# Kernel tuning notes

Hardware: AMD Instinct MI355X
Metric: run time of the kernel (lower is better)

## Reference

```python
import jax, jax.numpy as jnp
import numpy as np

D_MODEL, D_K, D_V, H = 1024, 64, 64, 16
B, N = 4, 2048


def setup_inputs() -> dict:
    key = jax.random.key(0)
    ks = jax.random.split(key, 11)
    s = 0.02
    return {
        "Q": jax.random.normal(ks[0], (B, N, D_MODEL), jnp.float32),
        "K": jax.random.normal(ks[1], (B, N, D_MODEL), jnp.float32),
        "V": jax.random.normal(ks[2], (B, N, D_MODEL), jnp.float32),
        # stacked per-head projection weights: [h, d_model, d_k]
        "Wq": jax.random.normal(ks[3], (H, D_MODEL, D_K), jnp.float32) * s,
        "bq": jax.random.normal(ks[4], (H, D_K), jnp.float32) * s,
        "Wk": jax.random.normal(ks[5], (H, D_MODEL, D_K), jnp.float32) * s,
        "bk": jax.random.normal(ks[6], (H, D_K), jnp.float32) * s,
        "Wv": jax.random.normal(ks[7], (H, D_MODEL, D_V), jnp.float32) * s,
        "bv": jax.random.normal(ks[8], (H, D_V), jnp.float32) * s,
        "Wo": jax.random.normal(ks[9], (H * D_V, D_MODEL), jnp.float32) * s,
        "bo": jax.random.normal(ks[10], (D_MODEL,), jnp.float32) * s,
        "apply_mask": 1,
    }


def reference(Q, K, V, Wq, bq, Wk, bk, Wv, bv, Wo, bo, apply_mask):
    # fused per-head projections: [b, h, n, d_k]
    q = jnp.einsum("bnd,hdk->bhnk", Q, Wq) + bq[None, :, None, :]
    k = jnp.einsum("bnd,hdk->bhnk", K, Wk) + bk[None, :, None, :]
    v = jnp.einsum("bnd,hdv->bhnv", V, Wv) + bv[None, :, None, :]
    scores = jnp.einsum("bhnk,bhmk->bhnm", q, k) / jnp.sqrt(
        jnp.asarray(D_K, q.dtype)
    )
    if apply_mask:
        n = Q.shape[1]
        causal = jnp.tril(jnp.ones((n, n), dtype=bool))
        scores = jnp.where(causal[None, None], scores, -jnp.inf)
    weights = jax.nn.softmax(scores, axis=-1)
    out = jnp.einsum("bhnm,bhmv->bhnv", weights, v)
    # concat heads: [b, n, h*d_v]
    out = out.transpose(0, 2, 1, 3).reshape(Q.shape[0], Q.shape[1], H * D_V)
    return out @ Wo + bo
```

## Files before the change

### kernel.cpp

```cpp
#include <hip/hip_runtime.h>
#include <hip/hip_bf16.h>

#define H 16
#define DM 1024
#define DK 64
#define B_ 4
#define N_ 2048

typedef __attribute__((ext_vector_type(8))) short bf16x8;
typedef __attribute__((ext_vector_type(4))) short s16x4;
typedef __attribute__((ext_vector_type(2))) unsigned int u32x2;
typedef __attribute__((ext_vector_type(4))) float f32x4;

static __device__ __forceinline__ short f2bs(float x) {
    __hip_bfloat16 b = __float2bfloat16(x);
    return *reinterpret_cast<short*>(&b);
}

static __device__ __forceinline__ void async16(const void* g, void* l) {
    __builtin_amdgcn_global_load_lds(
        (const __attribute__((address_space(1))) void*)g,
        (__attribute__((address_space(3))) void*)l, 16, 0, 0);
}

static __device__ __forceinline__ unsigned packbf(float lo, float hi) {
    return __builtin_amdgcn_perm(__float_as_uint(hi), __float_as_uint(lo), 0x07060302u);
}

__global__ __launch_bounds__(256) void prep_kernel(
    const float* __restrict__ Q, const float* __restrict__ K, const float* __restrict__ V,
    const float* __restrict__ Wq, const float* __restrict__ Wk,
    const float* __restrict__ Wv, const float* __restrict__ Wo,
    short* __restrict__ Qb, short* __restrict__ Kb, short* __restrict__ Vb,
    short* __restrict__ wqT, short* __restrict__ wkT,
    short* __restrict__ wvT, short* __restrict__ woT)
{
    int y = blockIdx.y;
    if (y < 3) {
        const float* s = (y == 0) ? Q : (y == 1) ? K : V;
        short* d = (y == 0) ? Qb : (y == 1) ? Kb : Vb;
        size_t i = ((size_t)blockIdx.x * 256 + threadIdx.x) * 8;
        f32x4 a = *(const f32x4*)(s + i);
        f32x4 b = *(const f32x4*)(s + i + 4);
        bf16x8 p;
        #pragma unroll
        for (int j = 0; j < 4; ++j) { p[j] = f2bs(a[j]); p[4 + j] = f2bs(b[j]); }
        *(bf16x8*)(d + i) = p;
        return;
    }
    if (blockIdx.x >= 1024) return;
    __shared__ float tile[64][65];
    int z = blockIdx.x >> 8;
    int bx = blockIdx.x & 255;
    int t = threadIdx.x;
    int tj = t & 63, ti = t >> 6;

    if (z < 3) {
        const float* src = (z == 0) ? Wq : (z == 1) ? Wk : Wv;
        short* dst = (z == 0) ? wqT : (z == 1) ? wkT : wvT;
        int h = bx >> 4;
        int dmt = bx & 15;
        #pragma unroll
        for (int r = 0; r < 16; ++r) {
            int i = r * 4 + ti;
            tile[i][tj] = src[((size_t)h * 1024 + dmt * 64 + i) * 64 + tj];
        }
        __syncthreads();
        #pragma unroll
        for (int r = 0; r < 16; ++r) {
            int dk = r * 4 + ti;
            dst[((size_t)h * 64 + dk) * 1024 + dmt * 64 + tj] = f2bs(tile[tj][dk]);
        }
    } else {
        int kt = bx >> 4;
        int nt = bx & 15;
        #pragma unroll
        for (int r = 0; r < 16; ++r) {
            int i = r * 4 + ti;
            tile[i][tj] = Wo[((size_t)kt * 64 + i) * 1024 + nt * 64 + tj];
        }
        __syncthreads();
        #pragma unroll
        for (int r = 0; r < 16; ++r) {
            int jn = r * 4 + ti;
            woT[((size_t)nt * 64 + jn) * 1024 + kt * 64 + tj] = f2bs(tile[tj][jn]);
        }
    }
}

static __device__ __forceinline__ void gemm_mainloop(
    const short* __restrict__ A, const short* __restrict__ BT,
    int rowM0, int colN0, char* lds, f32x4 (&acc)[4][4])
{
    int tid = threadIdx.x;
    int lane = tid & 63, w = tid >> 6;
    int l16 = lane & 15, quad = lane >> 4;
    int wm = w >> 1, wn = w & 1;
    int xg = (quad ^ ((l16 >> 1) & 3)) << 4;

    int r0 = w * 32 + (lane >> 2);
    int gsl = ((lane & 3) ^ ((lane >> 3) & 3)) << 4;
    int dst0 = w * 2048 + lane * 16;
    const char* Ag0 = (const char*)A + (size_t)(rowM0 + r0) * 2048 + gsl;
    const char* Ag1 = Ag0 + 16 * 2048;
    const char* Bg0 = (const char*)BT + (size_t)(colN0 + r0) * 2048 + gsl;
    const char* Bg1 = Bg0 + 16 * 2048;

    #pragma unroll
    for (int t = 0; t < 2; ++t) {
        size_t kb = (size_t)t * 64;
        char* As = lds + t * 16384;
        char* Bs = As + 8192;
        async16(Ag0 + kb, As + dst0);
        async16(Ag1 + kb, As + dst0 + 1024);
        async16(Bg0 + kb, Bs + dst0);
        async16(Bg1 + kb, Bs + dst0 + 1024);
    }

    int c0 = 0;
    int cr = 32768;
    for (int it = 0; it < 32; ++it) {
        if (it < 31) asm volatile("s_waitcnt vmcnt(4)" ::: "memory");
        else         asm volatile("s_waitcnt vmcnt(0)" ::: "memory");
        __builtin_amdgcn_s_barrier();
        __builtin_amdgcn_sched_barrier(0);

        if (it + 2 < 32) {
            size_t kb = (size_t)(it + 2) * 64;
            char* Aw = lds + cr;
            char* Bw = Aw + 8192;
            async16(Ag0 + kb, Aw + dst0);
            async16(Ag1 + kb, Aw + dst0 + 1024);
            async16(Bg0 + kb, Bw + dst0);
            async16(Bg1 + kb, Bw + dst0 + 1024);
        }
        __builtin_amdgcn_sched_barrier(0);

        const char* As = lds + c0;
        const char* Bs = As + 8192;
        bf16x8 a[4], b[4];
        #pragma unroll
        for (int i = 0; i < 4; ++i)
            a[i] = *(const bf16x8*)(As + (wm * 64 + i * 16 + l16) * 64 + xg);
        #pragma unroll
        for (int j = 0; j < 4; ++j)
            b[j] = *(const bf16x8*)(Bs + (wn * 64 + j * 16 + l16) * 64 + xg);
        #pragma unroll
        for (int i = 0; i < 4; ++i)
            #pragma unroll
            for (int j = 0; j < 4; ++j)
                acc[i][j] = __builtin_amdgcn_mfma_f32_16x16x32_bf16(a[i], b[j], acc[i][j], 0, 0, 0);

        c0 += 16384; if (c0 == 49152) c0 = 0;
        cr += 16384; if (cr == 49152) cr = 0;
    }
}

__global__ __launch_bounds__(256) void proj_gemm(
    const short* __restrict__ Qb, const short* __restrict__ Kb, const short* __restrict__ Vb,
    const short* __restrict__ wqT, const short* __restrict__ wkT, const short* __restrict__ wvT,
    const float* __restrict__ bq, const float* __restrict__ bk, const float* __restrict__ bv,
    short* __restrict__ qbuf, short* __restrict__ kbuf, short* __restrict__ vTbuf)
{
    __shared__ char lds[49152];
    int id = blockIdx.x;
    int xcd = id & 7;
    int k = id >> 3;
    int which = k >> 6;
    int rem = k & 63;
    int r = ((rem >> 3) << 3) | xcd;
    int c = rem & 7;

    const short* A  = (which == 0) ? Qb : (which == 1) ? Kb : Vb;
    const short* BT = (which == 0) ? wqT : (which == 1) ? wkT : wvT;
    const float* bias = (which == 0) ? bq : (which == 1) ? bk : bv;

    int rowM0 = r * 128;
    int colN0 = c * 128;

    f32x4 acc[4][4];
    #pragma unroll
    for (int i = 0; i < 4; ++i)
        #pragma unroll
        for (int j = 0; j < 4; ++j) acc[i][j] = (f32x4){0.f, 0.f, 0.f, 0.f};

    gemm_mainloop(A, BT, rowM0, colN0, lds, acc);

    int lane = threadIdx.x & 63, w = threadIdx.x >> 6;
    int l16 = lane & 15, quad = lane >> 4;
    int wm = w >> 1, wn = w & 1;

    if (which == 2) {
        #pragma unroll
        for (int j = 0; j < 4; ++j) {
            int col = colN0 + wn * 64 + j * 16 + l16;
            int hh = col >> 6, dv = col & 63;
            float bs = bias[col];
            #pragma unroll
            for (int i = 0; i < 4; ++i) {
                int rowb = rowM0 + wm * 64 + i * 16 + quad * 4;
                int bb = rowb >> 11, n0 = rowb & 2047;
                s16x4 pk;
                #pragma unroll
                for (int r2 = 0; r2 < 4; ++r2) pk[r2] = f2bs(acc[i][j][r2] + bs);
                *(s16x4*)(vTbuf + (((size_t)bb * H + hh) * DK + dv) * N_ + n0) = pk;
            }
        }
    } else {
        short* dst = (which == 0) ? qbuf : kbuf;
        float scl = (which == 0) ? 0.180336880f : 1.0f;
        #pragma unroll
        for (int j = 0; j < 4; ++j) {
            int col = colN0 + wn * 64 + j * 16 + l16;
            float bs = bias[col];
            #pragma unroll
            for (int i = 0; i < 4; ++i) {
                int rowb = rowM0 + wm * 64 + i * 16 + quad * 4;
                #pragma unroll
                for (int r2 = 0; r2 < 4; ++r2)
                    dst[(size_t)(rowb + r2) * 1024 + col] = f2bs((acc[i][j][r2] + bs) * scl);
            }
        }
    }
}

__global__ __launch_bounds__(256) void out_gemm(
    const short* __restrict__ obuf, const short* __restrict__ woT,
    const float* __restrict__ bo, float* __restrict__ out)
{
    __shared__ char lds[49152];
    int id = blockIdx.x;
    int xcd = id & 7;
    int k = id >> 3;
    int r = ((k >> 3) << 3) | xcd;
    int c = k & 7;

    int rowM0 = r * 128;
    int colN0 = c * 128;

    f32x4 acc[4][4];
    #pragma unroll
    for (int i = 0; i < 4; ++i)
        #pragma unroll
        for (int j = 0; j < 4; ++j) acc[i][j] = (f32x4){0.f, 0.f, 0.f, 0.f};

    gemm_mainloop(obuf, woT, rowM0, colN0, lds, acc);

    int lane = threadIdx.x & 63, w = threadIdx.x >> 6;
    int l16 = lane & 15, quad = lane >> 4;
    int wm = w >> 1, wn = w & 1;

    #pragma unroll
    for (int j = 0; j < 4; ++j) {
        int col = colN0 + wn * 64 + j * 16 + l16;
        float bs = bo[col];
        #pragma unroll
        for (int i = 0; i < 4; ++i) {
            int rowb = rowM0 + wm * 64 + i * 16 + quad * 4;
            #pragma unroll
            for (int r2 = 0; r2 < 4; ++r2)
                out[(size_t)(rowb + r2) * 1024 + col] = acc[i][j][r2] + bs;
        }
    }
}

__global__ __launch_bounds__(256) void flash_kernel(
    const short* __restrict__ qbuf, const short* __restrict__ kbuf, const short* __restrict__ vT,
    short* __restrict__ obuf, const int* __restrict__ amask)
{
    __shared__ short Ks[2][4096];
    __shared__ short Vs[2][4096];
    __shared__ char  plds[4][2048];

    int bid = blockIdx.x;
    int g = bid & 7, idx = bid >> 3;
    int bh = g * 8 + (idx >> 4);
    int xq = idx & 15;
    int b = bh >> 4, h = bh & 15;

    int tid = threadIdx.x;
    int lane = tid & 63, wave = tid >> 6;
    int l16 = lane & 15, quad = lane >> 4;
    int msk = amask[0];

    int i8 = lane >> 3, i7 = lane & 7;
    int sg = (i7 ^ i8) << 4;
    int pk0 = i8 * 4 + wave;
    int skey = wave * 16 + i8;
    int ldst = wave * 2048 + lane * 16;

    const char* kbase = (const char*)(kbuf + (size_t)b * 2048 * 1024 + h * 64);
    const char* vbase = (const char*)(vT + ((size_t)(b * 16 + h) * 64) * 2048);

    int m7 = l16 & 7;
    int g0 = (quad ^ m7) << 4;
    int g1 = ((4 | quad) ^ m7) << 4;

    char* pw = plds[wave];
    int prd0 = l16 * 128 + g0;
    int prd1 = l16 * 128 + g1;
    int pwa[4];
    #pragma unroll
    for (int r = 0; r < 4; ++r) {
        int row = quad * 4 + r;
        pwa[r] = row * 128 + (((l16 >> 1) ^ (row & 7)) << 4) + ((l16 & 1) << 3);
    }

    for (int pass = 0; pass < 2; ++pass) {
        int qt = pass ? (31 - xq) : xq;
        int qw = qt * 64 + wave * 16;
        int nkb = msk ? (qt + 1) : 32;

        const short* qp = qbuf + ((size_t)(b * 2048 + qw + l16)) * 1024 + h * 64;
        bf16x8 aq0 = *(const bf16x8*)(qp + quad * 8);
        bf16x8 aq1 = *(const bf16x8*)(qp + 32 + quad * 8);

        f32x4 o[4];
        float lsum[4];
        #pragma unroll
        for (int i = 0; i < 4; ++i) { o[i] = (f32x4){0.f, 0.f, 0.f, 0.f}; lsum[i] = 0.f; }

        async16(kbase + (size_t)pk0 * 2048 + sg, (char*)Ks[0] + ldst);
        async16(kbase + (size_t)(pk0 + 32) * 2048 + sg, (char*)Ks[0] + ldst + 1024);
        async16(vbase + (size_t)skey * 4096 + sg, (char*)Vs[0] + ldst);
        async16(vbase + (size_t)(skey + 8) * 4096 + sg, (char*)Vs[0] + ldst + 1024);

        for (int ib = 0; ib < nkb; ++ib) {
            __syncthreads();
            int cur = ib & 1;
            if (ib + 1 < nkb) {
                int nb = (ib + 1) & 1;
                size_t kb2 = (size_t)(ib + 1) * 64;
                async16(kbase + (kb2 + pk0) * 2048 + sg, (char*)Ks[nb] + ldst);
                async16(kbase + (kb2 + pk0 + 32) * 2048 + sg, (char*)Ks[nb] + ldst + 1024);
                async16(vbase + (size_t)skey * 4096 + kb2 * 2 + sg, (char*)Vs[nb] + ldst);
                async16(vbase + (size_t)(skey + 8) * 4096 + kb2 * 2 + sg, (char*)Vs[nb] + ldst + 1024);
            }
            int kb = ib * 64;

            f32x4 s[4];
            __builtin_amdgcn_s_setprio(1);
            #pragma unroll
            for (int nt = 0; nt < 4; ++nt) {
                const char* kr = (const char*)Ks[cur] + (nt * 16 + l16) * 128;
                bf16x8 b0 = *(const bf16x8*)(kr + g0);
                bf16x8 b1 = *(const bf16x8*)(kr + g1);
                f32x4 t = (f32x4){0.f, 0.f, 0.f, 0.f};
                t = __builtin_amdgcn_mfma_f32_16x16x32_bf16(aq0, b0, t, 0, 0, 0);
                t = __builtin_amdgcn_mfma_f32_16x16x32_bf16(aq1, b1, t, 0, 0, 0);
                s[nt] = t;
            }
            __builtin_amdgcn_s_setprio(0);

            if (msk && (kb + 63 > qw)) {
                #pragma unroll
                for (int r = 0; r < 4; ++r) {
                    int row = qw + quad * 4 + r;
                    #pragma unroll
                    for (int nt = 0; nt < 4; ++nt) {
                        int col = kb + l16 * 4 + nt;
                        if (col > row) s[nt][r] = -3e38f;
                    }
                }
            }

            __builtin_amdgcn_wave_barrier();
            #pragma unroll
            for (int r = 0; r < 4; ++r) {
                float p0 = __builtin_amdgcn_exp2f(s[0][r]);
                float p1 = __builtin_amdgcn_exp2f(s[1][r]);
                float p2 = __builtin_amdgcn_exp2f(s[2][r]);
                float p3 = __builtin_amdgcn_exp2f(s[3][r]);
                lsum[r] += (p0 + p1) + (p2 + p3);
                u32x2 pk;
                pk[0] = packbf(p0, p1);
                pk[1] = packbf(p2, p3);
                *(u32x2*)(pw + pwa[r]) = pk;
            }
            __builtin_amdgcn_wave_barrier();
            bf16x8 ap0 = *(const bf16x8*)(pw + prd0);
            bf16x8 ap1 = *(const bf16x8*)(pw + prd1);
            __builtin_amdgcn_wave_barrier();

            __builtin_amdgcn_s_setprio(1);
            #pragma unroll
            for (int vb = 0; vb < 4; ++vb) {
                const char* vr = (const char*)Vs[cur] + (vb * 16 + l16) * 128;
                bf16x8 v0 = *(const bf16x8*)(vr + g0);
                bf16x8 v1 = *(const bf16x8*)(vr + g1);
                o[vb] = __builtin_amdgcn_mfma_f32_16x16x32_bf16(ap0, v0, o[vb], 0, 0, 0);
                o[vb] = __builtin_amdgcn_mfma_f32_16x16x32_bf16(ap1, v1, o[vb], 0, 0, 0);
            }
            __builtin_amdgcn_s_setprio(0);
        }

        #pragma unroll
        for (int r = 0; r < 4; ++r) {
            float t = lsum[r];
            #pragma unroll
            for (int off = 1; off < 16; off <<= 1) t += __shfl_xor(t, off, 64);
            float inv = 1.0f / t;
            int row = qw + quad * 4 + r;
            #pragma unroll
            for (int vb = 0; vb < 4; ++vb)
                obuf[((size_t)(b * 2048 + row)) * 1024 + h * 64 + vb * 16 + l16] =
                    f2bs(o[vb][r] * inv);
        }
        __syncthreads();
    }
}

extern "C" void kernel_launch(void* const* d_in, const int* in_sizes, int n_in,
                              void* d_out, int out_size, void* d_ws, size_t ws_size,
                              hipStream_t stream)
{
    const float* Q  = (const float*)d_in[0];
    const float* K  = (const float*)d_in[1];
    const float* V  = (const float*)d_in[2];
    const float* Wq = (const float*)d_in[3];
    const float* bq = (const float*)d_in[4];
    const float* Wk = (const float*)d_in[5];
    const float* bk = (const float*)d_in[6];
    const float* Wv = (const float*)d_in[7];
    const float* bv = (const float*)d_in[8];
    const float* Wo = (const float*)d_in[9];
    const float* bo = (const float*)d_in[10];
    const int* amask = (const int*)d_in[11];
    float* out = (float*)d_out;

    char* ws = (char*)d_ws;
    const size_t SZ = (size_t)B_ * N_ * DM * sizeof(short);
    const size_t SZW = (size_t)H * DK * DM * sizeof(short);
    short* Qb    = (short*)ws; ws += SZ;
    short* Kb    = (short*)ws; ws += SZ;
    short* Vb    = (short*)ws; ws += SZ;
    short* qbuf  = (short*)ws; ws += SZ;
    short* kbuf  = (short*)ws; ws += SZ;
    short* vTbuf = (short*)ws; ws += SZ;
    short* wqT   = (short*)ws; ws += SZW;
    short* wkT   = (short*)ws; ws += SZW;
    short* wvT   = (short*)ws; ws += SZW;
    short* woT   = (short*)ws; ws += SZW;
    short* obuf  = Qb;

    prep_kernel<<<dim3(4096, 4), dim3(256), 0, stream>>>(Q, K, V, Wq, Wk, Wv, Wo,
                                                         Qb, Kb, Vb, wqT, wkT, wvT, woT);
    proj_gemm<<<dim3(1536), dim3(256), 0, stream>>>(Qb, Kb, Vb, wqT, wkT, wvT,
                                                    bq, bk, bv, qbuf, kbuf, vTbuf);
    flash_kernel<<<dim3(1024), dim3(256), 0, stream>>>(qbuf, kbuf, vTbuf, obuf, amask);
    out_gemm<<<dim3(512), dim3(256), 0, stream>>>(obuf, woT, bo, out);
}
```

Measured before the change: 303.3 us.

## Fuse fp32-to-bf16 input conversion into projection GEMM mainloop

Removes the separate pass that converted Q, K and V from fp32 to bf16 into workspace. The projection GEMM now loads fp32 A tiles into registers, converts them to bf16 and writes them to LDS, with a one-stage register prefetch. The weight B tiles still use async global-to-LDS loads. This cuts a full read/write round trip of the activations, but adds conversion ALU work and register pressure inside the GEMM loop, and doubles the A bytes fetched per tile.

Measured after the change: 335.6 us. 10.7% more time.

```diff
diff --git a/kernel.cpp b/kernel.cpp
--- a/kernel.cpp
+++ b/kernel.cpp
@@ -27,28 +27,12 @@
     return __builtin_amdgcn_perm(__float_as_uint(hi), __float_as_uint(lo), 0x07060302u);
 }
 
-__global__ __launch_bounds__(256) void prep_kernel(
-    const float* __restrict__ Q, const float* __restrict__ K, const float* __restrict__ V,
+__global__ __launch_bounds__(256) void prep_w(
     const float* __restrict__ Wq, const float* __restrict__ Wk,
     const float* __restrict__ Wv, const float* __restrict__ Wo,
-    short* __restrict__ Qb, short* __restrict__ Kb, short* __restrict__ Vb,
     short* __restrict__ wqT, short* __restrict__ wkT,
     short* __restrict__ wvT, short* __restrict__ woT)
 {
-    int y = blockIdx.y;
-    if (y < 3) {
-        const float* s = (y == 0) ? Q : (y == 1) ? K : V;
-        short* d = (y == 0) ? Qb : (y == 1) ? Kb : Vb;
-        size_t i = ((size_t)blockIdx.x * 256 + threadIdx.x) * 8;
-        f32x4 a = *(const f32x4*)(s + i);
-        f32x4 b = *(const f32x4*)(s + i + 4);
-        bf16x8 p;
-        #pragma unroll
-        for (int j = 0; j < 4; ++j) { p[j] = f2bs(a[j]); p[4 + j] = f2bs(b[j]); }
-        *(bf16x8*)(d + i) = p;
-        return;
-    }
-    if (blockIdx.x >= 1024) return;
     __shared__ float tile[64][65];
     int z = blockIdx.x >> 8;
     int bx = blockIdx.x & 255;
@@ -85,6 +69,97 @@
             int jn = r * 4 + ti;
             woT[((size_t)nt * 64 + jn) * 1024 + kt * 64 + tj] = f2bs(tile[tj][jn]);
         }
+    }
+}
+
+static __device__ __forceinline__ void gemm_mainloop_f32A(
+    const float* __restrict__ Af, const short* __restrict__ BT,
+    int rowM0, int colN0, char* lds, f32x4 (&acc)[4][4])
+{
+    int tid = threadIdx.x;
+    int lane = tid & 63, w = tid >> 6;
+    int l16 = lane & 15, quad = lane >> 4;
+    int wm = w >> 1, wn = w & 1;
+    int xg = (quad ^ ((l16 >> 1) & 3)) << 4;
+
+    int r0 = w * 32 + (lane >> 2);
+    int gsl = ((lane & 3) ^ ((lane >> 3) & 3)) << 4;
+    int dst0 = w * 2048 + lane * 16;
+    const char* Af0 = (const char*)Af + (size_t)(rowM0 + r0) * 4096 + gsl * 2;
+    const char* Af1 = Af0 + (size_t)16 * 4096;
+    const char* Bg0 = (const char*)BT + (size_t)(colN0 + r0) * 2048 + gsl;
+    const char* Bg1 = Bg0 + 16 * 2048;
+
+    f32x4 c00, c01, c10, c11;
+
+    c00 = *(const f32x4*)(Af0);
+    c01 = *(const f32x4*)(Af0 + 16);
+    c10 = *(const f32x4*)(Af1);
+    c11 = *(const f32x4*)(Af1 + 16);
+    async16(Bg0, lds + 8192 + dst0);
+    async16(Bg1, lds + 8192 + dst0 + 1024);
+    {
+        bf16x8 p0, p1;
+        #pragma unroll
+        for (int j = 0; j < 4; ++j) {
+            p0[j] = f2bs(c00[j]); p0[4 + j] = f2bs(c01[j]);
+            p1[j] = f2bs(c10[j]); p1[4 + j] = f2bs(c11[j]);
+        }
+        *(bf16x8*)(lds + dst0) = p0;
+        *(bf16x8*)(lds + dst0 + 1024) = p1;
+    }
+    c00 = *(const f32x4*)(Af0 + 128);
+    c01 = *(const f32x4*)(Af0 + 144);
+    c10 = *(const f32x4*)(Af1 + 128);
+    c11 = *(const f32x4*)(Af1 + 144);
+    async16(Bg0 + 64, lds + 16384 + 8192 + dst0);
+    async16(Bg1 + 64, lds + 16384 + 8192 + dst0 + 1024);
+
+    int o0 = 0, o1 = 16384, o2 = 32768;
+    for (int it = 0; it < 32; ++it) {
+        if (it < 31) asm volatile("s_waitcnt vmcnt(6) lgkmcnt(0)" ::: "memory");
+        else         asm volatile("s_waitcnt vmcnt(0) lgkmcnt(0)" ::: "memory");
+        __builtin_amdgcn_s_barrier();
+        __builtin_amdgcn_sched_barrier(0);
+
+        if (it + 1 < 32) {
+            bf16x8 p0, p1;
+            #pragma unroll
+            for (int j = 0; j < 4; ++j) {
+                p0[j] = f2bs(c00[j]); p0[4 + j] = f2bs(c01[j]);
+                p1[j] = f2bs(c10[j]); p1[4 + j] = f2bs(c11[j]);
+            }
+            *(bf16x8*)(lds + o1 + dst0) = p0;
+            *(bf16x8*)(lds + o1 + dst0 + 1024) = p1;
+        }
+        if (it + 2 < 32) {
+            int fo = (it + 2) * 128;
+            c00 = *(const f32x4*)(Af0 + fo);
+            c01 = *(const f32x4*)(Af0 + fo + 16);
+            c10 = *(const f32x4*)(Af1 + fo);
+            c11 = *(const f32x4*)(Af1 + fo + 16);
+            int bo2 = (it + 2) * 64;
+            async16(Bg0 + bo2, lds + o2 + 8192 + dst0);
+            async16(Bg1 + bo2, lds + o2 + 8192 + dst0 + 1024);
+        }
+        __builtin_amdgcn_sched_barrier(0);
+
+        const char* As = lds + o0;
+        const char* Bs = As + 8192;
+        bf16x8 a[4], b[4];
+        #pragma unroll
+        for (int i = 0; i < 4; ++i)
+            a[i] = *(const bf16x8*)(As + (wm * 64 + i * 16 + l16) * 64 + xg);
+        #pragma unroll
+        for (int j = 0; j < 4; ++j)
+            b[j] = *(const bf16x8*)(Bs + (wn * 64 + j * 16 + l16) * 64 + xg);
+        #pragma unroll
+        for (int i = 0; i < 4; ++i)
+            #pragma unroll
+            for (int j = 0; j < 4; ++j)
+                acc[i][j] = __builtin_amdgcn_mfma_f32_16x16x32_bf16(a[i], b[j], acc[i][j], 0, 0, 0);
+
+        int tmp = o0; o0 = o1; o1 = o2; o2 = tmp;
     }
 }
 
@@ -157,7 +232,7 @@
 }
 
 __global__ __launch_bounds__(256) void proj_gemm(
-    const short* __restrict__ Qb, const short* __restrict__ Kb, const short* __restrict__ Vb,
+    const float* __restrict__ Qf, const float* __restrict__ Kf, const float* __restrict__ Vf,
     const short* __restrict__ wqT, const short* __restrict__ wkT, const short* __restrict__ wvT,
     const float* __restrict__ bq, const float* __restrict__ bk, const float* __restrict__ bv,
     short* __restrict__ qbuf, short* __restrict__ kbuf, short* __restrict__ vTbuf)
@@ -171,7 +246,7 @@
     int r = ((rem >> 3) << 3) | xcd;
     int c = rem & 7;
 
-    const short* A  = (which == 0) ? Qb : (which == 1) ? Kb : Vb;
+    const float* A  = (which == 0) ? Qf : (which == 1) ? Kf : Vf;
     const short* BT = (which == 0) ? wqT : (which == 1) ? wkT : wvT;
     const float* bias = (which == 0) ? bq : (which == 1) ? bk : bv;
 
@@ -184,7 +259,7 @@
         #pragma unroll
         for (int j = 0; j < 4; ++j) acc[i][j] = (f32x4){0.f, 0.f, 0.f, 0.f};
 
-    gemm_mainloop(A, BT, rowM0, colN0, lds, acc);
+    gemm_mainloop_f32A(A, BT, rowM0, colN0, lds, acc);
 
     int lane = threadIdx.x & 63, w = threadIdx.x >> 6;
     int l16 = lane & 15, quad = lane >> 4;
@@ -431,9 +506,7 @@
     char* ws = (char*)d_ws;
     const size_t SZ = (size_t)B_ * N_ * DM * sizeof(short);
     const size_t SZW = (size_t)H * DK * DM * sizeof(short);
-    short* Qb    = (short*)ws; ws += SZ;
-    short* Kb    = (short*)ws; ws += SZ;
-    short* Vb    = (short*)ws; ws += SZ;
+    short* obuf  = (short*)ws; ws += SZ;
     short* qbuf  = (short*)ws; ws += SZ;
     short* kbuf  = (short*)ws; ws += SZ;
     short* vTbuf = (short*)ws; ws += SZ;
@@ -441,11 +514,9 @@
     short* wkT   = (short*)ws; ws += SZW;
     short* wvT   = (short*)ws; ws += SZW;
     short* woT   = (short*)ws; ws += SZW;
-    short* obuf  = Qb;
-
-    prep_kernel<<<dim3(4096, 4), dim3(256), 0, stream>>>(Q, K, V, Wq, Wk, Wv, Wo,
-                                                         Qb, Kb, Vb, wqT, wkT, wvT, woT);
-    proj_gemm<<<dim3(1536), dim3(256), 0, stream>>>(Qb, Kb, Vb, wqT, wkT, wvT,
+
+    prep_w<<<dim3(1024), dim3(256), 0, stream>>>(Wq, Wk, Wv, Wo, wqT, wkT, wvT, woT);
+    proj_gemm<<<dim3(1536), dim3(256), 0, stream>>>(Q, K, V, wqT, wkT, wvT,
                                                     bq, bk, bv, qbuf, kbuf, vTbuf);
     flash_kernel<<<dim3(1024), dim3(256), 0, stream>>>(qbuf, kbuf, vTbuf, obuf, amask);
     out_gemm<<<dim3(512), dim3(256), 0, stream>>>(obuf, woT, bo, out);
```

## Share K/V tiles between paired causal query tiles; drop XCD-aware block remap

Applied to the files above, without the earlier changes.

The flash kernel previously ran two sequential passes per block, for query tile xq and then 31-xq, loading K/V tiles from global memory in each pass. It now processes both query tiles in a single loop over key blocks. Each loaded K/V tile is reused for the short tile as well while it is still in range, which removes the duplicate K/V loads and the extra barriers. This costs more registers, since two sets of accumulators and Q fragments are live at once, and that may lower occupancy. Separately, the GEMM kernels drop the XCD-swizzled block index mapping in favour of a plain 2D/3D grid, which may hurt L2 locality across XCDs.

Measured after the change: 328.0 us. 1.08x slower.

```diff
diff --git a/kernel.cpp b/kernel.cpp
--- a/kernel.cpp
+++ b/kernel.cpp
@@ -163,20 +163,13 @@
     short* __restrict__ qbuf, short* __restrict__ kbuf, short* __restrict__ vTbuf)
 {
     __shared__ char lds[49152];
-    int id = blockIdx.x;
-    int xcd = id & 7;
-    int k = id >> 3;
-    int which = k >> 6;
-    int rem = k & 63;
-    int r = ((rem >> 3) << 3) | xcd;
-    int c = rem & 7;
-
+    int which = blockIdx.z;
     const short* A  = (which == 0) ? Qb : (which == 1) ? Kb : Vb;
     const short* BT = (which == 0) ? wqT : (which == 1) ? wkT : wvT;
     const float* bias = (which == 0) ? bq : (which == 1) ? bk : bv;
 
-    int rowM0 = r * 128;
-    int colN0 = c * 128;
+    int rowM0 = blockIdx.x * 128;
+    int colN0 = blockIdx.y * 128;
 
     f32x4 acc[4][4];
     #pragma unroll
@@ -229,14 +222,8 @@
     const float* __restrict__ bo, float* __restrict__ out)
 {
     __shared__ char lds[49152];
-    int id = blockIdx.x;
-    int xcd = id & 7;
-    int k = id >> 3;
-    int r = ((k >> 3) << 3) | xcd;
-    int c = k & 7;
-
-    int rowM0 = r * 128;
-    int colN0 = c * 128;
+    int rowM0 = blockIdx.x * 128;
+    int colN0 = blockIdx.y * 128;
 
     f32x4 acc[4][4];
     #pragma unroll
@@ -306,38 +293,47 @@
         pwa[r] = row * 128 + (((l16 >> 1) ^ (row & 7)) << 4) + ((l16 & 1) << 3);
     }
 
-    for (int pass = 0; pass < 2; ++pass) {
-        int qt = pass ? (31 - xq) : xq;
-        int qw = qt * 64 + wave * 16;
-        int nkb = msk ? (qt + 1) : 32;
-
-        const short* qp = qbuf + ((size_t)(b * 2048 + qw + l16)) * 1024 + h * 64;
-        bf16x8 aq0 = *(const bf16x8*)(qp + quad * 8);
-        bf16x8 aq1 = *(const bf16x8*)(qp + 32 + quad * 8);
-
-        f32x4 o[4];
-        float lsum[4];
-        #pragma unroll
-        for (int i = 0; i < 4; ++i) { o[i] = (f32x4){0.f, 0.f, 0.f, 0.f}; lsum[i] = 0.f; }
-
-        async16(kbase + (size_t)pk0 * 2048 + sg, (char*)Ks[0] + ldst);
-        async16(kbase + (size_t)(pk0 + 32) * 2048 + sg, (char*)Ks[0] + ldst + 1024);
-        async16(vbase + (size_t)skey * 4096 + sg, (char*)Vs[0] + ldst);
-        async16(vbase + (size_t)(skey + 8) * 4096 + sg, (char*)Vs[0] + ldst + 1024);
-
-        for (int ib = 0; ib < nkb; ++ib) {
-            __syncthreads();
-            int cur = ib & 1;
-            if (ib + 1 < nkb) {
-                int nb = (ib + 1) & 1;
-                size_t kb2 = (size_t)(ib + 1) * 64;
-                async16(kbase + (kb2 + pk0) * 2048 + sg, (char*)Ks[nb] + ldst);
-                async16(kbase + (kb2 + pk0 + 32) * 2048 + sg, (char*)Ks[nb] + ldst + 1024);
-                async16(vbase + (size_t)skey * 4096 + kb2 * 2 + sg, (char*)Vs[nb] + ldst);
-                async16(vbase + (size_t)(skey + 8) * 4096 + kb2 * 2 + sg, (char*)Vs[nb] + ldst + 1024);
-            }
-            int kb = ib * 64;
-
+    int qtA = xq, qtB = 31 - xq;
+    int qwA = qtA * 64 + wave * 16;
+    int qwB = qtB * 64 + wave * 16;
+    int nkbA = msk ? (qtA + 1) : 32;
+    int nkbB = msk ? (qtB + 1) : 32;
+
+    const short* qpA = qbuf + ((size_t)(b * 2048 + qwA + l16)) * 1024 + h * 64;
+    const short* qpB = qbuf + ((size_t)(b * 2048 + qwB + l16)) * 1024 + h * 64;
+    bf16x8 aqA0 = *(const bf16x8*)(qpA + quad * 8);
+    bf16x8 aqA1 = *(const bf16x8*)(qpA + 32 + quad * 8);
+    bf16x8 aqB0 = *(const bf16x8*)(qpB + quad * 8);
+    bf16x8 aqB1 = *(const bf16x8*)(qpB + 32 + quad * 8);
+
+    f32x4 oA[4], oB[4];
+    float lsA[4], lsB[4];
+    #pragma unroll
+    for (int i = 0; i < 4; ++i) {
+        oA[i] = (f32x4){0.f, 0.f, 0.f, 0.f};
+        oB[i] = (f32x4){0.f, 0.f, 0.f, 0.f};
+        lsA[i] = 0.f; lsB[i] = 0.f;
+    }
+
+    async16(kbase + (size_t)pk0 * 2048 + sg, (char*)Ks[0] + ldst);
+    async16(kbase + (size_t)(pk0 + 32) * 2048 + sg, (char*)Ks[0] + ldst + 1024);
+    async16(vbase + (size_t)skey * 4096 + sg, (char*)Vs[0] + ldst);
+    async16(vbase + (size_t)(skey + 8) * 4096 + sg, (char*)Vs[0] + ldst + 1024);
+
+    for (int ib = 0; ib < nkbB; ++ib) {
+        __syncthreads();
+        int cur = ib & 1;
+        if (ib + 1 < nkbB) {
+            int nb = (ib + 1) & 1;
+            size_t kb2 = (size_t)(ib + 1) * 64;
+            async16(kbase + (kb2 + pk0) * 2048 + sg, (char*)Ks[nb] + ldst);
+            async16(kbase + (kb2 + pk0 + 32) * 2048 + sg, (char*)Ks[nb] + ldst + 1024);
+            async16(vbase + (size_t)skey * 4096 + kb2 * 2 + sg, (char*)Vs[nb] + ldst);
+            async16(vbase + (size_t)(skey + 8) * 4096 + kb2 * 2 + sg, (char*)Vs[nb] + ldst + 1024);
+        }
+        int kb = ib * 64;
+
+        {
             f32x4 s[4];
             __builtin_amdgcn_s_setprio(1);
             #pragma unroll
@@ -346,16 +342,16 @@
                 bf16x8 b0 = *(const bf16x8*)(kr + g0);
                 bf16x8 b1 = *(const bf16x8*)(kr + g1);
                 f32x4 t = (f32x4){0.f, 0.f, 0.f, 0.f};
-                t = __builtin_amdgcn_mfma_f32_16x16x32_bf16(aq0, b0, t, 0, 0, 0);
-                t = __builtin_amdgcn_mfma_f32_16x16x32_bf16(aq1, b1, t, 0, 0, 0);
+                t = __builtin_amdgcn_mfma_f32_16x16x32_bf16(aqB0, b0, t, 0, 0, 0);
+                t = __builtin_amdgcn_mfma_f32_16x16x32_bf16(aqB1, b1, t, 0, 0, 0);
                 s[nt] = t;
             }
             __builtin_amdgcn_s_setprio(0);
 
-            if (msk && (kb + 63 > qw)) {
+            if (msk && (kb + 63 > qwB)) {
                 #pragma unroll
                 for (int r = 0; r < 4; ++r) {
-                    int row = qw + quad * 4 + r;
+                    int row = qwB + quad * 4 + r;
                     #pragma unroll
                     for (int nt = 0; nt < 4; ++nt) {
                         int col = kb + l16 * 4 + nt;
@@ -371,7 +367,7 @@
                 float p1 = __builtin_amdgcn_exp2f(s[1][r]);
                 float p2 = __builtin_amdgcn_exp2f(s[2][r]);
                 float p3 = __builtin_amdgcn_exp2f(s[3][r]);
-                lsum[r] += (p0 + p1) + (p2 + p3);
+                lsB[r] += (p0 + p1) + (p2 + p3);
                 u32x2 pk;
                 pk[0] = packbf(p0, p1);
                 pk[1] = packbf(p2, p3);
@@ -388,25 +384,93 @@
                 const char* vr = (const char*)Vs[cur] + (vb * 16 + l16) * 128;
                 bf16x8 v0 = *(const bf16x8*)(vr + g0);
                 bf16x8 v1 = *(const bf16x8*)(vr + g1);
-                o[vb] = __builtin_amdgcn_mfma_f32_16x16x32_bf16(ap0, v0, o[vb], 0, 0, 0);
-                o[vb] = __builtin_amdgcn_mfma_f32_16x16x32_bf16(ap1, v1, o[vb], 0, 0, 0);
+                oB[vb] = __builtin_amdgcn_mfma_f32_16x16x32_bf16(ap0, v0, oB[vb], 0, 0, 0);
+                oB[vb] = __builtin_amdgcn_mfma_f32_16x16x32_bf16(ap1, v1, oB[vb], 0, 0, 0);
             }
             __builtin_amdgcn_s_setprio(0);
         }
 
-        #pragma unroll
-        for (int r = 0; r < 4; ++r) {
-            float t = lsum[r];
-            #pragma unroll
-            for (int off = 1; off < 16; off <<= 1) t += __shfl_xor(t, off, 64);
-            float inv = 1.0f / t;
-            int row = qw + quad * 4 + r;
-            #pragma unroll
-            for (int vb = 0; vb < 4; ++vb)
-                obuf[((size_t)(b * 2048 + row)) * 1024 + h * 64 + vb * 16 + l16] =
-                    f2bs(o[vb][r] * inv);
-        }
-        __syncthreads();
+        if (ib < nkbA) {
+            f32x4 s[4];
+            __builtin_amdgcn_s_setprio(1);
+            #pragma unroll
+            for (int nt = 0; nt < 4; ++nt) {
+                const char* kr = (const char*)Ks[cur] + (nt * 16 + l16) * 128;
+                bf16x8 b0 = *(const bf16x8*)(kr + g0);
+                bf16x8 b1 = *(const bf16x8*)(kr + g1);
+                f32x4 t = (f32x4){0.f, 0.f, 0.f, 0.f};
+                t = __builtin_amdgcn_mfma_f32_16x16x32_bf16(aqA0, b0, t, 0, 0, 0);
+                t = __builtin_amdgcn_mfma_f32_16x16x32_bf16(aqA1, b1, t, 0, 0, 0);
+                s[nt] = t;
+            }
+            __builtin_amdgcn_s_setprio(0);
+
+            if (msk && (kb + 63 > qwA)) {
+                #pragma unroll
+                for (int r = 0; r < 4; ++r) {
+                    int row = qwA + quad * 4 + r;
+                    #pragma unroll
+                    for (int nt = 0; nt < 4; ++nt) {
+                        int col = kb + l16 * 4 + nt;
+                        if (col > row) s[nt][r] = -3e38f;
+                    }
+                }
+            }
+
+            __builtin_amdgcn_wave_barrier();
+            #pragma unroll
+            for (int r = 0; r < 4; ++r) {
+                float p0 = __builtin_amdgcn_exp2f(s[0][r]);
+                float p1 = __builtin_amdgcn_exp2f(s[1][r]);
+                float p2 = __builtin_amdgcn_exp2f(s[2][r]);
+                float p3 = __builtin_amdgcn_exp2f(s[3][r]);
+                lsA[r] += (p0 + p1) + (p2 + p3);
+                u32x2 pk;
+                pk[0] = packbf(p0, p1);
+                pk[1] = packbf(p2, p3);
+                *(u32x2*)(pw + pwa[r]) = pk;
+            }
+            __builtin_amdgcn_wave_barrier();
+            bf16x8 ap0 = *(const bf16x8*)(pw + prd0);
+            bf16x8 ap1 = *(const bf16x8*)(pw + prd1);
+            __builtin_amdgcn_wave_barrier();
+
+            __builtin_amdgcn_s_setprio(1);
+            #pragma unroll
+            for (int vb = 0; vb < 4; ++vb) {
+                const char* vr = (const char*)Vs[cur] + (vb * 16 + l16) * 128;
+                bf16x8 v0 = *(const bf16x8*)(vr + g0);
+                bf16x8 v1 = *(const bf16x8*)(vr + g1);
+                oA[vb] = __builtin_amdgcn_mfma_f32_16x16x32_bf16(ap0, v0, oA[vb], 0, 0, 0);
+                oA[vb] = __builtin_amdgcn_mfma_f32_16x16x32_bf16(ap1, v1, oA[vb], 0, 0, 0);
+            }
+            __builtin_amdgcn_s_setprio(0);
+        }
+    }
+
+    #pragma unroll
+    for (int r = 0; r < 4; ++r) {
+        float t = lsB[r];
+        #pragma unroll
+        for (int off = 1; off < 16; off <<= 1) t += __shfl_xor(t, off, 64);
+        float inv = 1.0f / t;
+        int row = qwB + quad * 4 + r;
+        #pragma unroll
+        for (int vb = 0; vb < 4; ++vb)
+            obuf[((size_t)(b * 2048 + row)) * 1024 + h * 64 + vb * 16 + l16] =
+                f2bs(oB[vb][r] * inv);
+    }
+    #pragma unroll
+    for (int r = 0; r < 4; ++r) {
+        float t = lsA[r];
+        #pragma unroll
+        for (int off = 1; off < 16; off <<= 1) t += __shfl_xor(t, off, 64);
+        float inv = 1.0f / t;
+        int row = qwA + quad * 4 + r;
+        #pragma unroll
+        for (int vb = 0; vb < 4; ++vb)
+            obuf[((size_t)(b * 2048 + row)) * 1024 + h * 64 + vb * 16 + l16] =
+                f2bs(oA[vb][r] * inv);
     }
 }
 
@@ -445,8 +509,8 @@
 
     prep_kernel<<<dim3(4096, 4), dim3(256), 0, stream>>>(Q, K, V, Wq, Wk, Wv, Wo,
                                                          Qb, Kb, Vb, wqT, wkT, wvT, woT);
-    proj_gemm<<<dim3(1536), dim3(256), 0, stream>>>(Qb, Kb, Vb, wqT, wkT, wvT,
-                                                    bq, bk, bv, qbuf, kbuf, vTbuf);
+    proj_gemm<<<dim3(64, 8, 3), dim3(256), 0, stream>>>(Qb, Kb, Vb, wqT, wkT, wvT,
+                                                        bq, bk, bv, qbuf, kbuf, vTbuf);
     flash_kernel<<<dim3(1024), dim3(256), 0, stream>>>(qbuf, kbuf, vTbuf, obuf, amask);
-    out_gemm<<<dim3(512), dim3(256), 0, stream>>>(obuf, woT, bo, out);
-}
+    out_gemm<<<dim3(64, 8), dim3(256), 0, stream>>>(obuf, woT, bo, out);
+}
```
